# Optimization experiments

Hardware: AMD Instinct MI355X
Metric: run time of the kernel (lower is better)

## Reference

```python
import jax, jax.numpy as jnp
import numpy as np

MODEL_DIM = 1024
NUM_HEAD = 16
HEAD_DIM = MODEL_DIM // NUM_HEAD
B, S = 2, 2048


def setup_inputs() -> dict:
    key = jax.random.key(0)
    ks = jax.random.split(key, 13)
    s = 1.0 / np.sqrt(MODEL_DIM)
    inp = {
        "q": jax.random.normal(ks[0], (B, S, MODEL_DIM), jnp.float32),
        "k": jax.random.normal(ks[1], (B, S, MODEL_DIM), jnp.float32),
        "v": jax.random.normal(ks[2], (B, S, MODEL_DIM), jnp.float32),
        "mask": jax.random.randint(ks[3], (S, S), 0, 2, jnp.int32),
        "w_q": jax.random.normal(ks[4], (MODEL_DIM, MODEL_DIM), jnp.float32) * s,
        "b_q": jax.random.normal(ks[5], (MODEL_DIM,), jnp.float32) * s,
        "w_k": jax.random.normal(ks[6], (MODEL_DIM, MODEL_DIM), jnp.float32) * s,
        "b_k": jax.random.normal(ks[7], (MODEL_DIM,), jnp.float32) * s,
        "w_v": jax.random.normal(ks[8], (MODEL_DIM, MODEL_DIM), jnp.float32) * s,
        "b_v": jax.random.normal(ks[9], (MODEL_DIM,), jnp.float32) * s,
        "w_o": jax.random.normal(ks[10], (MODEL_DIM, MODEL_DIM), jnp.float32) * s,
        "b_o": jax.random.normal(ks[11], (MODEL_DIM,), jnp.float32) * s,
    }
    return inp


def reference(q, k, v, mask, w_q, b_q, w_k, b_k, w_v, b_v, w_o, b_o):
    batch, seq_len, dim = q.shape
    # Linear projections (weights stored as [d_in, d_out])
    Q = q @ w_q + b_q
    K = k @ w_k + b_k
    V = v @ w_v + b_v
    # [B, H, S, Dh]
    Q = Q.reshape(batch, seq_len, NUM_HEAD, HEAD_DIM).transpose(0, 2, 1, 3)
    K = K.reshape(batch, seq_len, NUM_HEAD, HEAD_DIM).transpose(0, 2, 1, 3)
    V = V.reshape(batch, seq_len, NUM_HEAD, HEAD_DIM).transpose(0, 2, 1, 3)
    scores = jnp.einsum("bhqd,bhkd->bhqk", Q, K) / jnp.sqrt(
        jnp.asarray(HEAD_DIM, Q.dtype)
    )
    scores = jnp.where(mask == 0, jnp.asarray(-1e9, scores.dtype), scores)
    attn = jax.nn.softmax(scores, axis=-1)
    out = jnp.einsum("bhqk,bhkd->bhqd", attn, V)
    out = out.transpose(0, 2, 1, 3).reshape(batch, seq_len, dim)
    return out @ w_o + b_o
```

## Files before the change

### kernel.cpp

```cpp
#include <hip/hip_runtime.h>
#include <stdint.h>

typedef __bf16 bf16;
typedef __attribute__((ext_vector_type(4))) __bf16 bf16x4;
typedef __attribute__((ext_vector_type(8))) __bf16 bf16x8;
typedef __attribute__((ext_vector_type(4))) float f32x4;
typedef __attribute__((ext_vector_type(2))) float f32x2;

constexpr int S = 2048;
constexpr int D = 1024;
constexpr int H = 16;
constexpr int DH = 64;
constexpr int M = 4096;

constexpr float QSCALE = 0.18033688011112042f;

__device__ __forceinline__ void async16(void* lds, const void* g) {
  __builtin_amdgcn_global_load_lds(
      (const __attribute__((address_space(1))) void*)g,
      (__attribute__((address_space(3))) void*)lds, 16, 0, 0);
}

__global__ __launch_bounds__(256) void prep(
    const int* __restrict__ mask, uint64_t* __restrict__ MB,
    const float* __restrict__ q, const float* __restrict__ k,
    const float* __restrict__ v, bf16* __restrict__ qA, bf16* __restrict__ kA,
    bf16* __restrict__ vA, const float* __restrict__ Wq,
    const float* __restrict__ Wk, const float* __restrict__ Wv,
    const float* __restrict__ Wo, bf16* __restrict__ WTq,
    bf16* __restrict__ WTk, bf16* __restrict__ WTv, bf16* __restrict__ WoTh,
    bf16* __restrict__ WoTl) {
  __shared__ float T[64 * 68];
  const int bid = blockIdx.x;
  const int tid = threadIdx.x;

  if (bid < 16384) {
    const int gid = bid * 4 + (tid >> 6);
    const int lane = tid & 63;
    const int kt = gid >> 11;
    const int qq = gid & (S - 1);
    int mv = mask[(size_t)qq * S + kt * 64 + lane];
    uint64_t bits = __ballot(mv != 0);
    if (lane == 0) MB[(size_t)kt * S + qq] = bits;
    return;
  }

  if (bid < 28672) {
    const int idx = bid - 16384;
    const int z = idx >> 12;
    const int x = idx & 4095;
    const float* src = (z == 0) ? q : (z == 1) ? k : v;
    bf16* dst = (z == 0) ? qA : (z == 1) ? kA : vA;
    const size_t i = ((size_t)x * 256 + tid) * 4;
    f32x4 xv = *(const f32x4*)(src + i);
    bf16x4 o;
#pragma unroll
    for (int j = 0; j < 4; j++) o[j] = (bf16)xv[j];
    *(bf16x4*)(dst + i) = o;
    return;
  }

  const int idx = bid - 28672;
  const int z = idx >> 8;
  const int xy = idx & 255;
  const int n0 = (xy >> 4) * 64, k0 = (xy & 15) * 64;
  const float* W = (z == 0) ? Wq : (z == 1) ? Wk : (z == 2) ? Wv : Wo;
  const int lr = tid >> 4, lc = (tid & 15) * 4;
#pragma unroll
  for (int r = 0; r < 4; r++) {
    f32x4 vv = *(const f32x4*)(W + (size_t)(k0 + r * 16 + lr) * 1024 + n0 + lc);
    *(f32x4*)&T[(r * 16 + lr) * 68 + lc] = vv;
  }
  __syncthreads();
  const int nn = tid >> 3, kc = (tid & 7) * 8;
#pragma unroll
  for (int p = 0; p < 2; p++) {
    int n = p * 32 + nn;
    bf16x8 h, l;
#pragma unroll
    for (int j = 0; j < 8; j++) {
      float vv = T[(kc + j) * 68 + n];
      bf16 hh = (bf16)vv;
      h[j] = hh;
      l[j] = (bf16)(vv - (float)hh);
    }
    if (z < 3) {
      bf16* WT = (z == 0) ? WTq : (z == 1) ? WTk : WTv;
      *(bf16x8*)(WT + (size_t)(n0 + n) * 1024 + k0 + kc) = h;
    } else {
      *(bf16x8*)(WoTh + (size_t)(n0 + n) * 1024 + k0 + kc) = h;
      *(bf16x8*)(WoTl + (size_t)(n0 + n) * 1024 + k0 + kc) = l;
    }
  }
}

__global__ __launch_bounds__(256) void gemm_qkv(
    const bf16* __restrict__ Aq, const bf16* __restrict__ Ak,
    const bf16* __restrict__ Av, const bf16* __restrict__ WTq,
    const bf16* __restrict__ WTk, const bf16* __restrict__ WTv,
    const float* __restrict__ bq, const float* __restrict__ bk,
    const float* __restrict__ bv, bf16* __restrict__ Qb,
    bf16* __restrict__ Kb, bf16* __restrict__ VT) {
  __shared__ char smem[34816];

  const int z = blockIdx.z;
  const bf16* A = (z == 0) ? Aq : (z == 1) ? Ak : Av;
  const bf16* WT = (z == 0) ? WTq : (z == 1) ? WTk : WTv;
  const float* bias = (z == 0) ? bq : (z == 1) ? bk : bv;
  const float oscale = (z == 0) ? QSCALE : 1.0f;

  const int tid = threadIdx.x;
  const int bn = blockIdx.x * 128;
  const int bm = blockIdx.y * 128;
  const int wv = tid >> 6;
  const int lane = tid & 63;
  const int quad = lane >> 4;
  const int lo = lane & 15;
  const int wm = (wv >> 1) * 64;
  const int wn = (wv & 1) * 64;

  f32x4 acc[4][4];
#pragma unroll
  for (int i = 0; i < 4; i++)
#pragma unroll
    for (int j = 0; j < 4; j++) acc[i][j] = {0.f, 0.f, 0.f, 0.f};

  const int rloc = lane >> 3;
  const int gx = (lane & 7) ^ rloc;
  const int rx = (lo & 7);

  for (int kt = 0; kt < 16; ++kt) {
#pragma unroll
    for (int j = 0; j < 4; j++) {
      int ch = wv * 4 + j;
      async16(smem + ch * 1024,
              A + (size_t)(bm + ch * 8 + rloc) * 1024 + kt * 64 + gx * 8);
      async16(smem + 16384 + ch * 1024,
              WT + (size_t)(bn + ch * 8 + rloc) * 1024 + kt * 64 + gx * 8);
    }
    __syncthreads();

#pragma unroll
    for (int ks = 0; ks < 2; ks++) {
      bf16x8 af[4], bfr[4];
#pragma unroll
      for (int mi = 0; mi < 4; mi++)
        af[mi] = *(const bf16x8*)(smem + (wm + mi * 16 + lo) * 128 +
                                  (((ks * 4 + quad) ^ rx) * 16));
#pragma unroll
      for (int ni = 0; ni < 4; ni++)
        bfr[ni] = *(const bf16x8*)(smem + 16384 + (wn + ni * 16 + lo) * 128 +
                                   (((ks * 4 + quad) ^ rx) * 16));
#pragma unroll
      for (int mi = 0; mi < 4; mi++)
#pragma unroll
        for (int ni = 0; ni < 4; ni++)
          acc[mi][ni] = __builtin_amdgcn_mfma_f32_16x16x32_bf16(
              af[mi], bfr[ni], acc[mi][ni], 0, 0, 0);
    }
    __syncthreads();
  }

  const int b = bm >> 11;
  const int srow0 = bm & (S - 1);

  if (z == 2) {
#pragma unroll
    for (int mi = 0; mi < 4; mi++)
#pragma unroll
      for (int ni = 0; ni < 4; ni++) {
        int col = bn + wn + ni * 16 + lo;
        int h = col >> 6, dh = col & 63;
        float bvv = bias[col];
        bf16x4 t;
#pragma unroll
        for (int r = 0; r < 4; r++) t[r] = (bf16)(acc[mi][ni][r] + bvv);
        int s0 = srow0 + wm + mi * 16 + quad * 4;
        *(bf16x4*)&VT[(((size_t)(b * H + h)) * DH + dh) * S + s0] = t;
      }
    return;
  }

  bf16* T = (bf16*)smem;
#pragma unroll
  for (int mi = 0; mi < 4; mi++)
#pragma unroll
    for (int ni = 0; ni < 4; ni++) {
      int col = wn + ni * 16 + lo;
      float bvv = bias[bn + col];
#pragma unroll
      for (int r = 0; r < 4; r++) {
        int row = wm + mi * 16 + quad * 4 + r;
        T[row * 136 + col] = (bf16)((acc[mi][ni][r] + bvv) * oscale);
      }
    }
  __syncthreads();
  bf16* out = (z == 0) ? Qb : Kb;
  const int rr = tid >> 1;
  const int half = tid & 1;
  const int h = (bn >> 6) + half;
  bf16* gp = out + (((size_t)(b * H + h)) * S + srow0 + rr) * DH;
#pragma unroll
  for (int j = 0; j < 8; j++)
    *(bf16x8*)(gp + j * 8) = *(const bf16x8*)&T[rr * 136 + half * 64 + j * 8];
}

__global__ __launch_bounds__(256) void gemm_o(
    const bf16* __restrict__ AOh, const bf16* __restrict__ AOl,
    const bf16* __restrict__ Wh, const bf16* __restrict__ Wl,
    float* __restrict__ dout, float* __restrict__ P1) {
  __shared__ char smem[32768];

  const int z = blockIdx.z;
  float* out = (z == 0) ? dout : P1;

  const int tid = threadIdx.x;
  const int bn = blockIdx.x * 128;
  const int bm = blockIdx.y * 128;
  const int wv = tid >> 6;
  const int lane = tid & 63;
  const int quad = lane >> 4;
  const int lo = lane & 15;
  const int wm = (wv >> 1) * 64;
  const int wn = (wv & 1) * 64;

  f32x4 acc[4][4];
#pragma unroll
  for (int i = 0; i < 4; i++)
#pragma unroll
    for (int j = 0; j < 4; j++) acc[i][j] = {0.f, 0.f, 0.f, 0.f};

  const int pl = lane >> 3;
  const int uu = lane & 7;
  const int srow = pl * 2 + (uu & 1);
  const int sg = (uu >> 1) ^ (pl & 3);
  const int uread = (((quad ^ ((lo >> 1) & 3)) << 1) | (lo & 1)) * 16;
  const int aoff = (lo >> 1) * 128 + uread;

  for (int kt = z * 16; kt < z * 16 + 16; ++kt) {
#pragma unroll
    for (int t = 0; t < 4; t++) {
      const bf16* src = (t == 0) ? AOh : (t == 1) ? AOl : (t == 2) ? Wh : Wl;
      int rb = (t < 2) ? bm : bn;
#pragma unroll
      for (int j = 0; j < 2; j++) {
        int c = wv * 2 + j;
        async16(smem + t * 8192 + c * 1024,
                src + (size_t)(rb + c * 16 + srow) * 1024 + kt * 32 + sg * 8);
      }
    }
    __syncthreads();

    bf16x8 ah[4], al[4], bh[4], bl[4];
    const char* ap = smem + wm * 64 + aoff;
    const char* bp = smem + 16384 + wn * 64 + aoff;
#pragma unroll
    for (int mi = 0; mi < 4; mi++) {
      ah[mi] = *(const bf16x8*)(ap + mi * 1024);
      al[mi] = *(const bf16x8*)(ap + 8192 + mi * 1024);
    }
#pragma unroll
    for (int ni = 0; ni < 4; ni++) {
      bh[ni] = *(const bf16x8*)(bp + ni * 1024);
      bl[ni] = *(const bf16x8*)(bp + 8192 + ni * 1024);
    }
#pragma unroll
    for (int mi = 0; mi < 4; mi++)
#pragma unroll
      for (int ni = 0; ni < 4; ni++) {
        acc[mi][ni] = __builtin_amdgcn_mfma_f32_16x16x32_bf16(ah[mi], bh[ni], acc[mi][ni], 0, 0, 0);
        acc[mi][ni] = __builtin_amdgcn_mfma_f32_16x16x32_bf16(ah[mi], bl[ni], acc[mi][ni], 0, 0, 0);
        acc[mi][ni] = __builtin_amdgcn_mfma_f32_16x16x32_bf16(al[mi], bh[ni], acc[mi][ni], 0, 0, 0);
      }
    __syncthreads();
  }

#pragma unroll
  for (int mi = 0; mi < 4; mi++)
#pragma unroll
    for (int ni = 0; ni < 4; ni++) {
      int col = bn + wn + ni * 16 + lo;
#pragma unroll
      for (int r = 0; r < 4; r++) {
        int row = bm + wm + mi * 16 + quad * 4 + r;
        out[(size_t)row * 1024 + col] = acc[mi][ni][r];
      }
    }
}

__global__ __launch_bounds__(256) void combine_o(const float* __restrict__ P1,
                                                 const float* __restrict__ bias,
                                                 float* __restrict__ out) {
  const size_t i = ((size_t)blockIdx.x * 256 + threadIdx.x) * 4;
  f32x4 a = *(const f32x4*)(out + i);
  f32x4 p = *(const f32x4*)(P1 + i);
  f32x4 bv = *(const f32x4*)(bias + ((int)i & 1023));
  f32x4 r;
#pragma unroll
  for (int j = 0; j < 4; j++) r[j] = a[j] + p[j] + bv[j];
  *(f32x4*)(out + i) = r;
}

__global__ __launch_bounds__(512) void attn_kernel(
    const bf16* __restrict__ Qg, const bf16* __restrict__ Kg,
    const bf16* __restrict__ VTg, const uint64_t* __restrict__ MB,
    bf16* __restrict__ AOh, bf16* __restrict__ AOl) {
  __shared__ char smem[49152];

  const int tid = threadIdx.x;
  const int wv = tid >> 6;
  const int lane = tid & 63;
  const int quad = lane >> 4;
  const int lo = lane & 15;

  const int lin = blockIdx.x;
  const int bh = (lin & 7) * 4 + ((lin >> 3) & 3);
  const int qt = lin >> 5;
  const int qbase = qt * 128 + wv * 16;
  const size_t base = (size_t)bh * S * DH;
  bf16* Pw = (bf16*)(smem + 32768 + wv * 2048);
  const int xm = (lo & 7) << 1;

  const int c0 = wv * 2;
  const int rloc = lane >> 3;
  const int gx = (lane & 7) ^ rloc;
  const int rx = lo & 7;

  bf16x8 qf[2];
  {
    const bf16* qp = Qg + base + (size_t)(qbase + lo) * DH + quad * 8;
    qf[0] = *(const bf16x8*)qp;
    qf[1] = *(const bf16x8*)(qp + 32);
  }

  f32x4 Oacc[4];
#pragma unroll
  for (int j = 0; j < 4; j++) Oacc[j] = {0.f, 0.f, 0.f, 0.f};
  f32x2 lp = {0.f, 0.f};

#define STAGE(kt_, buf_)                                                       \
  {                                                                            \
    _Pragma("unroll") for (int j = 0; j < 2; j++) {                            \
      int c = c0 + j;                                                          \
      if (c < 8) {                                                             \
        async16((buf_) + c * 1024,                                             \
                Kg + base + (size_t)((kt_)*64 + c * 8 + rloc) * 64 + gx * 8);  \
      } else {                                                                 \
        int cv = c - 8;                                                        \
        async16((buf_) + 8192 + cv * 1024,                                     \
                VTg + base + (size_t)(cv * 8 + rloc) * S + (kt_)*64 + gx * 8); \
      }                                                                        \
    }                                                                          \
  }

  STAGE(0, smem);
  uint64_t mcur = MB[(size_t)0 * S + qbase + lo];

  for (int kt = 0; kt < 32; ++kt) {
    const char* cur = smem + (kt & 1) * 16384;

    uint64_t m0 = mcur >> (quad * 4);
    uint32_t mw[2] = {(uint32_t)m0, (uint32_t)(m0 >> 32)};

    __syncthreads();
    if (kt + 1 < 32) {
      STAGE(kt + 1, smem + ((kt + 1) & 1) * 16384);
      mcur = MB[(size_t)(kt + 1) * S + qbase + lo];
    }

    const char* Kls = cur;
    const char* Vls = cur + 8192;

    f32x4 sacc[4];
#pragma unroll
    for (int mi = 0; mi < 4; mi++) sacc[mi] = {0.f, 0.f, 0.f, 0.f};
    __builtin_amdgcn_s_setprio(1);
#pragma unroll
    for (int mi = 0; mi < 4; mi++) {
      bf16x8 k0 = *(const bf16x8*)(Kls + (mi * 16 + lo) * 128 + ((quad ^ rx) * 16));
      bf16x8 k1 = *(const bf16x8*)(Kls + (mi * 16 + lo) * 128 + (((4 + quad) ^ rx) * 16));
      sacc[mi] = __builtin_amdgcn_mfma_f32_16x16x32_bf16(k0, qf[0], sacc[mi], 0, 0, 0);
      sacc[mi] = __builtin_amdgcn_mfma_f32_16x16x32_bf16(k1, qf[1], sacc[mi], 0, 0, 0);
    }
    __builtin_amdgcn_s_setprio(0);

#pragma unroll
    for (int mi = 0; mi < 4; mi++) {
      bf16x4 t;
#pragma unroll
      for (int r = 0; r < 4; r++) {
        float p = __builtin_amdgcn_exp2f(sacc[mi][r]);
        int ext = __builtin_amdgcn_sbfe((int)mw[mi >> 1], ((mi & 1) << 4) + r, 1);
        p = __builtin_bit_cast(float, __builtin_bit_cast(int, p) & ext);
        lp[r & 1] += p;
        t[r] = (bf16)p;
      }
      *(bf16x4*)&Pw[lo * 64 + (((mi * 4 + quad) ^ xm) * 4)] = t;
    }

    __builtin_amdgcn_s_setprio(1);
#pragma unroll
    for (int kk = 0; kk < 2; kk++) {
      int g16 = kk * 8 + quad * 2;
      bf16x8 pa = *(const bf16x8*)&Pw[lo * 64 + ((g16 ^ xm) * 4)];
#pragma unroll
      for (int ni = 0; ni < 4; ni++) {
        bf16x8 vb = *(const bf16x8*)(Vls + (ni * 16 + lo) * 128 +
                                     (((kk * 4 + quad) ^ rx) * 16));
        Oacc[ni] = __builtin_amdgcn_mfma_f32_16x16x32_bf16(pa, vb, Oacc[ni], 0, 0, 0);
      }
    }
    __builtin_amdgcn_s_setprio(0);
  }
#undef STAGE

  float lpart = lp[0] + lp[1];
  lpart += __shfl_xor(lpart, 16);
  lpart += __shfl_xor(lpart, 32);

  const int b = bh >> 4, h = bh & (H - 1);
#pragma unroll
  for (int r = 0; r < 4; r++) {
    float inv = 1.0f / __shfl(lpart, quad * 4 + r);
    int q = qbase + quad * 4 + r;
    size_t rowoff = (size_t)(b * S + q) * D + h * DH;
#pragma unroll
    for (int ni = 0; ni < 4; ni++) {
      float o = Oacc[ni][r] * inv;
      bf16 hi = (bf16)o;
      AOh[rowoff + ni * 16 + lo] = hi;
      AOl[rowoff + ni * 16 + lo] = (bf16)(o - (float)hi);
    }
  }
}

extern "C" void kernel_launch(void* const* d_in, const int* in_sizes, int n_in,
                              void* d_out, int out_size, void* d_ws,
                              size_t ws_size, hipStream_t stream) {
  const float* q = (const float*)d_in[0];
  const float* k = (const float*)d_in[1];
  const float* v = (const float*)d_in[2];
  const int* mask = (const int*)d_in[3];
  const float* w_q = (const float*)d_in[4];
  const float* b_q = (const float*)d_in[5];
  const float* w_k = (const float*)d_in[6];
  const float* b_k = (const float*)d_in[7];
  const float* w_v = (const float*)d_in[8];
  const float* b_v = (const float*)d_in[9];
  const float* w_o = (const float*)d_in[10];
  const float* b_o = (const float*)d_in[11];

  char* w = (char*)d_ws;
  const size_t MiB = 1ull << 20;
  bf16* Qb = (bf16*)w;
  bf16* Kb = (bf16*)(w + 8 * MiB);
  bf16* VT = (bf16*)(w + 16 * MiB);
  bf16* qA = (bf16*)(w + 24 * MiB);
  bf16* kA = (bf16*)(w + 32 * MiB);
  bf16* vA = (bf16*)(w + 40 * MiB);
  bf16* AOh = (bf16*)(w + 24 * MiB);
  bf16* AOl = (bf16*)(w + 32 * MiB);
  float* P1 = (float*)w;
  bf16* WTq = (bf16*)(w + 48 * MiB);
  bf16* WTk = (bf16*)(w + 50 * MiB);
  bf16* WTv = (bf16*)(w + 52 * MiB);
  bf16* WoTh = (bf16*)(w + 54 * MiB);
  bf16* WoTl = (bf16*)(w + 56 * MiB);
  uint64_t* MBits = (uint64_t*)(w + 58 * MiB);

  prep<<<29696, 256, 0, stream>>>(mask, MBits, q, k, v, qA, kA, vA, w_q, w_k,
                                  w_v, w_o, WTq, WTk, WTv, WoTh, WoTl);
  gemm_qkv<<<dim3(8, 32, 3), 256, 0, stream>>>(qA, kA, vA, WTq, WTk, WTv, b_q,
                                               b_k, b_v, Qb, Kb, VT);
  attn_kernel<<<dim3(512), 512, 0, stream>>>(Qb, Kb, VT, MBits, AOh, AOl);
  gemm_o<<<dim3(8, 32, 2), 256, 0, stream>>>(AOh, AOl, WoTh, WoTl,
                                             (float*)d_out, P1);
  combine_o<<<4096, 256, 0, stream>>>(P1, b_o, (float*)d_out);
}
```

Measured before the change: 279.6 us.

## Drop split-K in output GEMM and fuse bias add, removing combine kernel

The output projection no longer splits K across two grid slices that each write a full fp32 partial buffer followed by a separate combine kernel. Each block now runs the full K loop with 512 threads: eight waves each own a 32x64 sub-tile, and each wave loads one 16-row chunk per operand. The bias is added in the epilogue. This removes the partial-sum write and read traffic and one kernel launch. In exchange the grid shrinks to 256 blocks, each with a longer serial K loop.

```diff
diff --git a/kernel.cpp b/kernel.cpp
--- a/kernel.cpp
+++ b/kernel.cpp
@@ -205,14 +205,11 @@
     *(bf16x8*)(gp + j * 8) = *(const bf16x8*)&T[rr * 136 + half * 64 + j * 8];
 }
 
-__global__ __launch_bounds__(256) void gemm_o(
+__global__ __launch_bounds__(512) void gemm_o(
     const bf16* __restrict__ AOh, const bf16* __restrict__ AOl,
     const bf16* __restrict__ Wh, const bf16* __restrict__ Wl,
-    float* __restrict__ dout, float* __restrict__ P1) {
+    const float* __restrict__ bias, float* __restrict__ out) {
   __shared__ char smem[32768];
-
-  const int z = blockIdx.z;
-  float* out = (z == 0) ? dout : P1;
 
   const int tid = threadIdx.x;
   const int bn = blockIdx.x * 128;
@@ -221,12 +218,12 @@
   const int lane = tid & 63;
   const int quad = lane >> 4;
   const int lo = lane & 15;
-  const int wm = (wv >> 1) * 64;
+  const int wm = (wv >> 1) * 32;
   const int wn = (wv & 1) * 64;
 
-  f32x4 acc[4][4];
-#pragma unroll
-  for (int i = 0; i < 4; i++)
+  f32x4 acc[2][4];
+#pragma unroll
+  for (int i = 0; i < 2; i++)
 #pragma unroll
     for (int j = 0; j < 4; j++) acc[i][j] = {0.f, 0.f, 0.f, 0.f};
 
@@ -237,25 +234,21 @@
   const int uread = (((quad ^ ((lo >> 1) & 3)) << 1) | (lo & 1)) * 16;
   const int aoff = (lo >> 1) * 128 + uread;
 
-  for (int kt = z * 16; kt < z * 16 + 16; ++kt) {
+  for (int kt = 0; kt < 32; ++kt) {
 #pragma unroll
     for (int t = 0; t < 4; t++) {
       const bf16* src = (t == 0) ? AOh : (t == 1) ? AOl : (t == 2) ? Wh : Wl;
       int rb = (t < 2) ? bm : bn;
-#pragma unroll
-      for (int j = 0; j < 2; j++) {
-        int c = wv * 2 + j;
-        async16(smem + t * 8192 + c * 1024,
-                src + (size_t)(rb + c * 16 + srow) * 1024 + kt * 32 + sg * 8);
-      }
+      async16(smem + t * 8192 + wv * 1024,
+              src + (size_t)(rb + wv * 16 + srow) * 1024 + kt * 32 + sg * 8);
     }
     __syncthreads();
 
-    bf16x8 ah[4], al[4], bh[4], bl[4];
+    bf16x8 ah[2], al[2], bh[4], bl[4];
     const char* ap = smem + wm * 64 + aoff;
     const char* bp = smem + 16384 + wn * 64 + aoff;
 #pragma unroll
-    for (int mi = 0; mi < 4; mi++) {
+    for (int mi = 0; mi < 2; mi++) {
       ah[mi] = *(const bf16x8*)(ap + mi * 1024);
       al[mi] = *(const bf16x8*)(ap + 8192 + mi * 1024);
     }
@@ -265,7 +258,7 @@
       bl[ni] = *(const bf16x8*)(bp + 8192 + ni * 1024);
     }
 #pragma unroll
-    for (int mi = 0; mi < 4; mi++)
+    for (int mi = 0; mi < 2; mi++)
 #pragma unroll
       for (int ni = 0; ni < 4; ni++) {
         acc[mi][ni] = __builtin_amdgcn_mfma_f32_16x16x32_bf16(ah[mi], bh[ni], acc[mi][ni], 0, 0, 0);
@@ -276,29 +269,17 @@
   }
 
 #pragma unroll
-  for (int mi = 0; mi < 4; mi++)
+  for (int mi = 0; mi < 2; mi++)
 #pragma unroll
     for (int ni = 0; ni < 4; ni++) {
       int col = bn + wn + ni * 16 + lo;
+      float bvv = bias[col];
 #pragma unroll
       for (int r = 0; r < 4; r++) {
         int row = bm + wm + mi * 16 + quad * 4 + r;
-        out[(size_t)row * 1024 + col] = acc[mi][ni][r];
-      }
-    }
-}
-
-__global__ __launch_bounds__(256) void combine_o(const float* __restrict__ P1,
-                                                 const float* __restrict__ bias,
-                                                 float* __restrict__ out) {
-  const size_t i = ((size_t)blockIdx.x * 256 + threadIdx.x) * 4;
-  f32x4 a = *(const f32x4*)(out + i);
-  f32x4 p = *(const f32x4*)(P1 + i);
-  f32x4 bv = *(const f32x4*)(bias + ((int)i & 1023));
-  f32x4 r;
-#pragma unroll
-  for (int j = 0; j < 4; j++) r[j] = a[j] + p[j] + bv[j];
-  *(f32x4*)(out + i) = r;
+        out[(size_t)row * 1024 + col] = acc[mi][ni][r] + bvv;
+      }
+    }
 }
 
 __global__ __launch_bounds__(512) void attn_kernel(
@@ -460,7 +441,6 @@
   bf16* vA = (bf16*)(w + 40 * MiB);
   bf16* AOh = (bf16*)(w + 24 * MiB);
   bf16* AOl = (bf16*)(w + 32 * MiB);
-  float* P1 = (float*)w;
   bf16* WTq = (bf16*)(w + 48 * MiB);
   bf16* WTk = (bf16*)(w + 50 * MiB);
   bf16* WTv = (bf16*)(w + 52 * MiB);
@@ -473,7 +453,6 @@
   gemm_qkv<<<dim3(8, 32, 3), 256, 0, stream>>>(qA, kA, vA, WTq, WTk, WTv, b_q,
                                                b_k, b_v, Qb, Kb, VT);
   attn_kernel<<<dim3(512), 512, 0, stream>>>(Qb, Kb, VT, MBits, AOh, AOl);
-  gemm_o<<<dim3(8, 32, 2), 256, 0, stream>>>(AOh, AOl, WoTh, WoTl,
-                                             (float*)d_out, P1);
-  combine_o<<<4096, 256, 0, stream>>>(P1, b_o, (float*)d_out);
-}
+  gemm_o<<<dim3(8, 32), 512, 0, stream>>>(AOh, AOl, WoTh, WoTl, b_o,
+                                          (float*)d_out);
+}
```

Result: no change. 275.1 us (-1.6%).
